# Kernel optimization log

Hardware: AMD Instinct MI355X
Metric: run time of the kernel (lower is better)

## Reference

```python
import jax, jax.numpy as jnp
import numpy as np


def _gru_cell(x, h, wih, whh, bih, bhh):
    """PyTorch GRUCell semantics. x:[B,2] h:[B,2] wih/whh:[6,2] bih/bhh:[6]."""
    gi = x @ wih.T + bih  # [B,6]
    gh = h @ whh.T + bhh  # [B,6]
    i_r, i_z, i_n = jnp.split(gi, 3, axis=1)
    h_r, h_z, h_n = jnp.split(gh, 3, axis=1)
    r = jax.nn.sigmoid(i_r + h_r)
    z = jax.nn.sigmoid(i_z + h_z)
    n = jnp.tanh(i_n + r * h_n)
    return (1.0 - z) * n + z * h


def setup_inputs() -> dict:
    key = jax.random.key(0)
    ks = jax.random.split(key, 13)
    B = 1048576
    s = 0.5  # small init scale for stable gates
    return {
        "x": jax.random.normal(ks[0], (B, 19), dtype=jnp.float32),
        "up_wih": jax.random.normal(ks[1], (6, 2), dtype=jnp.float32) * s,
        "up_whh": jax.random.normal(ks[2], (6, 2), dtype=jnp.float32) * s,
        "up_bih": jax.random.normal(ks[3], (6,), dtype=jnp.float32) * s,
        "up_bhh": jax.random.normal(ks[4], (6,), dtype=jnp.float32) * s,
        "down_wih": jax.random.normal(ks[5], (6, 2), dtype=jnp.float32) * s,
        "down_whh": jax.random.normal(ks[6], (6, 2), dtype=jnp.float32) * s,
        "down_bih": jax.random.normal(ks[7], (6,), dtype=jnp.float32) * s,
        "down_bhh": jax.random.normal(ks[8], (6,), dtype=jnp.float32) * s,
        "obs_w": jax.random.normal(ks[9], (2, 7), dtype=jnp.float32) * s,
        "obs_b": jax.random.normal(ks[10], (2,), dtype=jnp.float32) * s,
        "out_w": jax.random.normal(ks[11], (1, 2), dtype=jnp.float32) * s,
        "out_b": jax.random.normal(ks[12], (1,), dtype=jnp.float32) * s,
    }


def reference(x, up_wih, up_whh, up_bih, up_bhh,
              down_wih, down_whh, down_bih, down_bhh,
              obs_w, obs_b, out_w, out_b):
    B = x.shape[0]
    obs = x[:, :5]                       # [B,5]
    j = x[:, 5:12]                       # [B,7]
    jd = x[:, 12:19]                     # [B,7]
    jcat = jnp.stack([j, jd], axis=-1)   # [B,7,2] per-joint (pos, vel)
    steps = jnp.swapaxes(jcat, 0, 1)     # [7,B,2]

    # up pass: scan r_up over the 7 joints, collecting hidden states
    h0 = jnp.zeros((B, 2), dtype=x.dtype)

    def up_step(h, inp):
        h_new = _gru_cell(inp, h, up_wih, up_whh, up_bih, up_bhh)
        return h_new, h_new

    h_last, h_up = jax.lax.scan(up_step, h0, steps)  # h_up: [7,B,2]

    # mix observation with final up hidden state
    h = jnp.concatenate([obs, h_last], axis=1) @ obs_w.T + obs_b  # [B,2]

    # down pass: scan r_down over stored up states, emitting actions
    def down_step(h, hu):
        h_new = _gru_cell(hu, h, down_wih, down_whh, down_bih, down_bhh)
        act = h_new @ out_w.T + out_b  # [B,1]
        return h_new, act

    _, acts = jax.lax.scan(down_step, h, h_up)  # [7,B,1]
    return jnp.swapaxes(acts, 0, 1)  # [B,7,1]
```

## Files before the change

### kernel.cpp

```cpp
#include <hip/hip_runtime.h>

#define TPB 256

__device__ __forceinline__ float fast_rcp(float x) { return __builtin_amdgcn_rcpf(x); }
__device__ __forceinline__ float sigm(float x) { return fast_rcp(1.0f + __expf(-x)); }
__device__ __forceinline__ float ftanh(float x) { return 1.0f - 2.0f * fast_rcp(__expf(2.0f * x) + 1.0f); }

#define GRU_STEP(WIH, WHH, BIH, BHH, X0, X1, H0, H1)                          \
  {                                                                            \
    const float x0_ = (X0), x1_ = (X1);                                        \
    float pre0 = fmaf(WIH[0], x0_, fmaf(WIH[1], x1_, BIH[0] + BHH[0]));        \
    float pre1 = fmaf(WIH[2], x0_, fmaf(WIH[3], x1_, BIH[1] + BHH[1]));        \
    float pre2 = fmaf(WIH[4], x0_, fmaf(WIH[5], x1_, BIH[2] + BHH[2]));        \
    float pre3 = fmaf(WIH[6], x0_, fmaf(WIH[7], x1_, BIH[3] + BHH[3]));        \
    float gin0 = fmaf(WIH[8], x0_, fmaf(WIH[9], x1_, BIH[4]));                 \
    float gin1 = fmaf(WIH[10], x0_, fmaf(WIH[11], x1_, BIH[5]));               \
    float r0 = sigm(fmaf(WHH[0], H0, fmaf(WHH[1], H1, pre0)));                 \
    float r1 = sigm(fmaf(WHH[2], H0, fmaf(WHH[3], H1, pre1)));                 \
    float z0 = sigm(fmaf(WHH[4], H0, fmaf(WHH[5], H1, pre2)));                 \
    float z1 = sigm(fmaf(WHH[6], H0, fmaf(WHH[7], H1, pre3)));                 \
    float ghn0 = fmaf(WHH[8], H0, fmaf(WHH[9], H1, BHH[4]));                   \
    float ghn1 = fmaf(WHH[10], H0, fmaf(WHH[11], H1, BHH[5]));                 \
    float n0 = ftanh(fmaf(r0, ghn0, gin0));                                    \
    float n1 = ftanh(fmaf(r1, ghn1, gin1));                                    \
    float omz0 = 1.0f - z0, zh0 = z0 * (H0);                                   \
    float omz1 = 1.0f - z1, zh1 = z1 * (H1);                                   \
    H0 = fmaf(n0, omz0, zh0);                                                  \
    H1 = fmaf(n1, omz1, zh1);                                                  \
  }

__global__ __launch_bounds__(TPB) void rec_policy_kernel(
    const float* __restrict__ x,
    const float* __restrict__ up_wih, const float* __restrict__ up_whh,
    const float* __restrict__ up_bih, const float* __restrict__ up_bhh,
    const float* __restrict__ down_wih, const float* __restrict__ down_whh,
    const float* __restrict__ down_bih, const float* __restrict__ down_bhh,
    const float* __restrict__ obs_w, const float* __restrict__ obs_b,
    const float* __restrict__ out_w, const float* __restrict__ out_b,
    float* __restrict__ out, int B) {
  __shared__ float sx[TPB * 19];
  __shared__ float sout[TPB * 7];

  const int tid = threadIdx.x;
  const int base = blockIdx.x * TPB;
  const int rows = min(TPB, B - base);

  if (rows == TPB) {
    const float4* src = (const float4*)(x + (size_t)base * 19);
    float4* dst = (float4*)sx;
#pragma unroll
    for (int i = tid; i < TPB * 19 / 4; i += TPB) dst[i] = src[i];
  } else {
    for (int i = tid; i < rows * 19; i += TPB) sx[i] = x[(size_t)base * 19 + i];
  }
  __syncthreads();

  if (tid < rows) {
    const float* xr = sx + tid * 19;
    float hu[14];

    {
      float h0 = 0.f, h1 = 0.f;
#pragma unroll
      for (int t = 0; t < 7; ++t) {
        GRU_STEP(up_wih, up_whh, up_bih, up_bhh, xr[5 + t], xr[12 + t], h0, h1);
        hu[2 * t] = h0;
        hu[2 * t + 1] = h1;
      }
    }

    float h0, h1;
    {
      float acc0 = obs_b[0], acc1 = obs_b[1];
#pragma unroll
      for (int k = 0; k < 5; ++k) {
        float c = xr[k];
        acc0 = fmaf(c, obs_w[k], acc0);
        acc1 = fmaf(c, obs_w[7 + k], acc1);
      }
      acc0 = fmaf(hu[12], obs_w[5], fmaf(hu[13], obs_w[6], acc0));
      acc1 = fmaf(hu[12], obs_w[12], fmaf(hu[13], obs_w[13], acc1));
      h0 = acc0;
      h1 = acc1;
    }

    {
      const float ow0 = out_w[0], ow1 = out_w[1], ob = out_b[0];
#pragma unroll
      for (int t = 0; t < 7; ++t) {
        GRU_STEP(down_wih, down_whh, down_bih, down_bhh, hu[2 * t], hu[2 * t + 1],
                 h0, h1);
        sout[tid * 7 + t] = fmaf(ow0, h0, fmaf(ow1, h1, ob));
      }
    }
  }
  __syncthreads();

  if (rows == TPB) {
    float4* dst = (float4*)(out + (size_t)base * 7);
    const float4* src = (const float4*)sout;
#pragma unroll
    for (int i = tid; i < TPB * 7 / 4; i += TPB) dst[i] = src[i];
  } else {
    for (int i = tid; i < rows * 7; i += TPB) out[(size_t)base * 7 + i] = sout[i];
  }
}

extern "C" void kernel_launch(void* const* d_in, const int* in_sizes, int n_in,
                              void* d_out, int out_size, void* d_ws, size_t ws_size,
                              hipStream_t stream) {
  const float* x        = (const float*)d_in[0];
  const float* up_wih   = (const float*)d_in[1];
  const float* up_whh   = (const float*)d_in[2];
  const float* up_bih   = (const float*)d_in[3];
  const float* up_bhh   = (const float*)d_in[4];
  const float* down_wih = (const float*)d_in[5];
  const float* down_whh = (const float*)d_in[6];
  const float* down_bih = (const float*)d_in[7];
  const float* down_bhh = (const float*)d_in[8];
  const float* obs_w    = (const float*)d_in[9];
  const float* obs_b    = (const float*)d_in[10];
  const float* out_w    = (const float*)d_in[11];
  const float* out_b    = (const float*)d_in[12];
  float* out = (float*)d_out;

  const int B = in_sizes[0] / 19;
  const int blocks = (B + TPB - 1) / TPB;
  rec_policy_kernel<<<blocks, TPB, 0, stream>>>(
      x, up_wih, up_whh, up_bih, up_bhh, down_wih, down_whh, down_bih, down_bhh,
      obs_w, obs_b, out_w, out_b, out, B);
}
```

Measured before the change: 156.2 us.

## Prescale GRU weights for exp2 gates, peel first step, write output directly

Folds the -log2(e) and 2*log2(e) factors into the GRU weights and biases once per thread, so each sigmoid and tanh uses a raw exp2 with no extra multiply. The first up-pass step is peeled out, since h starts at zero and the hidden-to-hidden terms drop away. The shared-memory output staging and its second barrier are removed, and each thread writes its 7 outputs straight to global memory. The direct per-thread writes use a 28-byte stride and are less coalesced than the old float4 copy, so store traffic may get worse.

```diff
diff --git a/kernel.cpp b/kernel.cpp
--- a/kernel.cpp
+++ b/kernel.cpp
@@ -1,33 +1,77 @@
 #include <hip/hip_runtime.h>
 
 #define TPB 256
+#define L2E 1.4426950408889634f
 
 __device__ __forceinline__ float fast_rcp(float x) { return __builtin_amdgcn_rcpf(x); }
-__device__ __forceinline__ float sigm(float x) { return fast_rcp(1.0f + __expf(-x)); }
-__device__ __forceinline__ float ftanh(float x) { return 1.0f - 2.0f * fast_rcp(__expf(2.0f * x) + 1.0f); }
+__device__ __forceinline__ float exp2_fast(float x) { return __builtin_amdgcn_exp2f(x); }
+__device__ __forceinline__ float sigm2(float s) { return fast_rcp(1.0f + exp2_fast(s)); }
+__device__ __forceinline__ float tanh2(float y) {
+  return fmaf(-2.0f, fast_rcp(exp2_fast(y) + 1.0f), 1.0f);
+}
 
-#define GRU_STEP(WIH, WHH, BIH, BHH, X0, X1, H0, H1)                          \
-  {                                                                            \
-    const float x0_ = (X0), x1_ = (X1);                                        \
-    float pre0 = fmaf(WIH[0], x0_, fmaf(WIH[1], x1_, BIH[0] + BHH[0]));        \
-    float pre1 = fmaf(WIH[2], x0_, fmaf(WIH[3], x1_, BIH[1] + BHH[1]));        \
-    float pre2 = fmaf(WIH[4], x0_, fmaf(WIH[5], x1_, BIH[2] + BHH[2]));        \
-    float pre3 = fmaf(WIH[6], x0_, fmaf(WIH[7], x1_, BIH[3] + BHH[3]));        \
-    float gin0 = fmaf(WIH[8], x0_, fmaf(WIH[9], x1_, BIH[4]));                 \
-    float gin1 = fmaf(WIH[10], x0_, fmaf(WIH[11], x1_, BIH[5]));               \
-    float r0 = sigm(fmaf(WHH[0], H0, fmaf(WHH[1], H1, pre0)));                 \
-    float r1 = sigm(fmaf(WHH[2], H0, fmaf(WHH[3], H1, pre1)));                 \
-    float z0 = sigm(fmaf(WHH[4], H0, fmaf(WHH[5], H1, pre2)));                 \
-    float z1 = sigm(fmaf(WHH[6], H0, fmaf(WHH[7], H1, pre3)));                 \
-    float ghn0 = fmaf(WHH[8], H0, fmaf(WHH[9], H1, BHH[4]));                   \
-    float ghn1 = fmaf(WHH[10], H0, fmaf(WHH[11], H1, BHH[5]));                 \
-    float n0 = ftanh(fmaf(r0, ghn0, gin0));                                    \
-    float n1 = ftanh(fmaf(r1, ghn1, gin1));                                    \
-    float omz0 = 1.0f - z0, zh0 = z0 * (H0);                                   \
-    float omz1 = 1.0f - z1, zh1 = z1 * (H1);                                   \
-    H0 = fmaf(n0, omz0, zh0);                                                  \
-    H1 = fmaf(n1, omz1, zh1);                                                  \
+struct GruW {
+  float wrz[8], urz[8], brz[4];
+  float wn[4], un[4], bin[2], bhn[2];
+};
+
+__device__ __forceinline__ void load_gru(const float* __restrict__ wih,
+                                         const float* __restrict__ whh,
+                                         const float* __restrict__ bih,
+                                         const float* __restrict__ bhh, GruW& g) {
+#pragma unroll
+  for (int i = 0; i < 8; ++i) {
+    g.wrz[i] = wih[i] * (-L2E);
+    g.urz[i] = whh[i] * (-L2E);
   }
+#pragma unroll
+  for (int i = 0; i < 4; ++i) {
+    g.brz[i] = (bih[i] + bhh[i]) * (-L2E);
+    g.wn[i] = wih[8 + i] * (2.0f * L2E);
+    g.un[i] = whh[8 + i] * (2.0f * L2E);
+  }
+#pragma unroll
+  for (int i = 0; i < 2; ++i) {
+    g.bin[i] = bih[4 + i] * (2.0f * L2E);
+    g.bhn[i] = bhh[4 + i] * (2.0f * L2E);
+  }
+}
+
+template <bool FIRST>
+__device__ __forceinline__ void gru_step(const GruW& g, float x0, float x1,
+                                         float& h0, float& h1) {
+  float pr0 = fmaf(g.wrz[0], x0, fmaf(g.wrz[1], x1, g.brz[0]));
+  float pr1 = fmaf(g.wrz[2], x0, fmaf(g.wrz[3], x1, g.brz[1]));
+  float pz0 = fmaf(g.wrz[4], x0, fmaf(g.wrz[5], x1, g.brz[2]));
+  float pz1 = fmaf(g.wrz[6], x0, fmaf(g.wrz[7], x1, g.brz[3]));
+  float gin0 = fmaf(g.wn[0], x0, fmaf(g.wn[1], x1, g.bin[0]));
+  float gin1 = fmaf(g.wn[2], x0, fmaf(g.wn[3], x1, g.bin[1]));
+  float sr0, sr1, sz0, sz1, ghn0, ghn1;
+  if constexpr (FIRST) {
+    sr0 = pr0; sr1 = pr1; sz0 = pz0; sz1 = pz1;
+    ghn0 = g.bhn[0]; ghn1 = g.bhn[1];
+  } else {
+    sr0 = fmaf(g.urz[0], h0, fmaf(g.urz[1], h1, pr0));
+    sr1 = fmaf(g.urz[2], h0, fmaf(g.urz[3], h1, pr1));
+    sz0 = fmaf(g.urz[4], h0, fmaf(g.urz[5], h1, pz0));
+    sz1 = fmaf(g.urz[6], h0, fmaf(g.urz[7], h1, pz1));
+    ghn0 = fmaf(g.un[0], h0, fmaf(g.un[1], h1, g.bhn[0]));
+    ghn1 = fmaf(g.un[2], h0, fmaf(g.un[3], h1, g.bhn[1]));
+  }
+  float r0 = sigm2(sr0), r1 = sigm2(sr1);
+  float z0 = sigm2(sz0), z1 = sigm2(sz1);
+  float n0 = tanh2(fmaf(r0, ghn0, gin0));
+  float n1 = tanh2(fmaf(r1, ghn1, gin1));
+  float omz0 = 1.0f - z0, omz1 = 1.0f - z1;
+  if constexpr (FIRST) {
+    h0 = n0 * omz0;
+    h1 = n1 * omz1;
+  } else {
+    float zh0 = z0 * h0, zh1 = z1 * h1;
+    h0 = fmaf(n0, omz0, zh0);
+    h1 = fmaf(n1, omz1, zh1);
+  }
+}
 
 __global__ __launch_bounds__(TPB) void rec_policy_kernel(
     const float* __restrict__ x,
@@ -39,7 +83,6 @@
     const float* __restrict__ out_w, const float* __restrict__ out_b,
     float* __restrict__ out, int B) {
   __shared__ float sx[TPB * 19];
-  __shared__ float sout[TPB * 7];
 
   const int tid = threadIdx.x;
   const int base = blockIdx.x * TPB;
@@ -48,7 +91,6 @@
   if (rows == TPB) {
     const float4* src = (const float4*)(x + (size_t)base * 19);
     float4* dst = (float4*)sx;
-#pragma unroll
     for (int i = tid; i < TPB * 19 / 4; i += TPB) dst[i] = src[i];
   } else {
     for (int i = tid; i < rows * 19; i += TPB) sx[i] = x[(size_t)base * 19 + i];
@@ -59,17 +101,21 @@
     const float* xr = sx + tid * 19;
     float hu[14];
 
+    float h0, h1;
     {
-      float h0 = 0.f, h1 = 0.f;
+      GruW ug;
+      load_gru(up_wih, up_whh, up_bih, up_bhh, ug);
+      gru_step<true>(ug, xr[5], xr[12], h0, h1);
+      hu[0] = h0;
+      hu[1] = h1;
 #pragma unroll
-      for (int t = 0; t < 7; ++t) {
-        GRU_STEP(up_wih, up_whh, up_bih, up_bhh, xr[5 + t], xr[12 + t], h0, h1);
+      for (int t = 1; t < 7; ++t) {
+        gru_step<false>(ug, xr[5 + t], xr[12 + t], h0, h1);
         hu[2 * t] = h0;
         hu[2 * t + 1] = h1;
       }
     }
 
-    float h0, h1;
     {
       float acc0 = obs_b[0], acc1 = obs_b[1];
 #pragma unroll
@@ -85,24 +131,16 @@
     }
 
     {
+      GruW dg;
+      load_gru(down_wih, down_whh, down_bih, down_bhh, dg);
       const float ow0 = out_w[0], ow1 = out_w[1], ob = out_b[0];
+      float* orow = out + ((size_t)base + tid) * 7;
 #pragma unroll
       for (int t = 0; t < 7; ++t) {
-        GRU_STEP(down_wih, down_whh, down_bih, down_bhh, hu[2 * t], hu[2 * t + 1],
-                 h0, h1);
-        sout[tid * 7 + t] = fmaf(ow0, h0, fmaf(ow1, h1, ob));
+        gru_step<false>(dg, hu[2 * t], hu[2 * t + 1], h0, h1);
+        orow[t] = fmaf(ow0, h0, fmaf(ow1, h1, ob));
       }
     }
-  }
-  __syncthreads();
-
-  if (rows == TPB) {
-    float4* dst = (float4*)(out + (size_t)base * 7);
-    const float4* src = (const float4*)sout;
-#pragma unroll
-    for (int i = tid; i < TPB * 7 / 4; i += TPB) dst[i] = src[i];
-  } else {
-    for (int i = tid; i < rows * 7; i += TPB) out[(size_t)base * 7 + i] = sout[i];
   }
 }
 
```

After: 155.8 us. No clear change (-0.2%).
